# Optimization experiments

Hardware: AMD Instinct MI355X
Metric: run time of the kernel (lower is better)

The kernel has to match this reference:

```python
import jax, jax.numpy as jnp
import numpy as np

D_MODEL = 512
N_HEAD = 8
D_FF = 2048
HEAD = D_MODEL // N_HEAD
B, S = 2, 4096
LN_EPS = 1e-5


def _layernorm(x, g, b):
    mu = jnp.mean(x, axis=-1, keepdims=True)
    var = jnp.mean(jnp.square(x - mu), axis=-1, keepdims=True)
    return (x - mu) * jax.lax.rsqrt(var + LN_EPS) * g + b


def setup_inputs() -> dict:
    key = jax.random.key(0)
    ks = jax.random.split(key, 12)
    s = 0.02
    inp = {
        "src": jax.random.normal(ks[0], (B, S, D_MODEL), dtype=jnp.float32),
        "mask": jnp.ones((B, S, S), dtype=jnp.float32),
        "Wq": jax.random.normal(ks[1], (D_MODEL, D_MODEL), dtype=jnp.float32) * s,
        "bq": jnp.zeros((D_MODEL,), dtype=jnp.float32),
        "Wk": jax.random.normal(ks[2], (D_MODEL, D_MODEL), dtype=jnp.float32) * s,
        "bk": jnp.zeros((D_MODEL,), dtype=jnp.float32),
        "Wv": jax.random.normal(ks[3], (D_MODEL, D_MODEL), dtype=jnp.float32) * s,
        "bv": jnp.zeros((D_MODEL,), dtype=jnp.float32),
        "Wo": jax.random.normal(ks[4], (D_MODEL, D_MODEL), dtype=jnp.float32) * s,
        "bo": jnp.zeros((D_MODEL,), dtype=jnp.float32),
        "W1": jax.random.normal(ks[5], (D_FF, D_MODEL), dtype=jnp.float32) * s,
        "b1": jnp.zeros((D_FF,), dtype=jnp.float32),
        "W2": jax.random.normal(ks[6], (D_MODEL, D_FF), dtype=jnp.float32) * s,
        "b2": jnp.zeros((D_MODEL,), dtype=jnp.float32),
        "ln1_g": jnp.ones((D_MODEL,), dtype=jnp.float32),
        "ln1_b": jnp.zeros((D_MODEL,), dtype=jnp.float32),
        "ln2_g": jnp.ones((D_MODEL,), dtype=jnp.float32),
        "ln2_b": jnp.zeros((D_MODEL,), dtype=jnp.float32),
    }
    return inp


def reference(src, mask, Wq, bq, Wk, bk, Wv, bv, Wo, bo, W1, b1, W2, b2,
              ln1_g, ln1_b, ln2_g, ln2_b):
    # --- multi-head self-attention (chunk/cat == head split on last dim) ---
    def heads(x, W, b):
        y = x @ W.T + b  # [B,S,D]
        return y.reshape(B, S, N_HEAD, HEAD)
    Q = heads(src, Wq, bq)
    K = heads(src, Wk, bk)
    V = heads(src, Wv, bv)
    score = jnp.einsum('bihd,bjhd->bhij', Q, K) / jnp.sqrt(jnp.float32(HEAD))
    score = score + ((1.0 - mask) * -1e9)[:, None, :, :]
    attn = jax.nn.softmax(score, axis=-1)
    ctx = jnp.einsum('bhij,bjhd->bihd', attn, V).reshape(B, S, D_MODEL)
    sa = ctx @ Wo.T + bo
    # --- residual + LN1 ---
    x = _layernorm(src + sa, ln1_g, ln1_b)
    # --- FFN (relu) + residual + LN2 ---
    ff = jax.nn.relu(x @ W1.T + b1) @ W2.T + b2
    return _layernorm(x + ff, ln2_g, ln2_b)
```

## Files before the change

### kernel.cpp

```cpp
#include <hip/hip_runtime.h>
#include <cstdint>
#include <cstddef>

#define DM   512
#define SQL  4096
#define NHE  8
#define HDM  64
#define DFF  2048
#define NB   2

typedef unsigned short u16t;
typedef __attribute__((ext_vector_type(8))) __bf16 bf16x8;
typedef __attribute__((ext_vector_type(4))) float f32x4;
typedef __attribute__((ext_vector_type(8))) unsigned short us8;
typedef __attribute__((ext_vector_type(4))) unsigned short us4;
typedef __attribute__((ext_vector_type(4))) short s16x4;

extern "C" __device__ float __ocml_native_exp2_f32(float);
__device__ inline float ex2(float x) { return __ocml_native_exp2_f32(x); }

__device__ inline f32x4 mfma16(bf16x8 a, bf16x8 b, f32x4 c) {
    return __builtin_amdgcn_mfma_f32_16x16x32_bf16(a, b, c, 0, 0, 0);
}
__device__ inline f32x4 mfma16k16(s16x4 a, s16x4 b, f32x4 c) {
    return __builtin_amdgcn_mfma_f32_16x16x16bf16_1k(a, b, c, 0, 0, 0);
}

__device__ inline void load_lds16(const void* g, void* l) {
    __builtin_amdgcn_global_load_lds(
        (const __attribute__((address_space(1))) unsigned int*)g,
        (__attribute__((address_space(3))) unsigned int*)l, 16, 0, 0);
}

__device__ inline u16t f2bf(float x) {
    union { float f; unsigned int u; } v; v.f = x;
    unsigned int r = v.u + 0x7fffu + ((v.u >> 16) & 1u);
    return (u16t)(r >> 16);
}

__device__ inline unsigned int pk_bf2(float lo, float hi) {
    union { float f; unsigned int u; } a, b;
    a.f = lo; b.f = hi;
    return __builtin_amdgcn_perm(b.u + 0x8000u, a.u + 0x8000u, 0x07060302u);
}

__device__ inline void store_out(float* C, size_t idx, float v) { C[idx] = v; }
__device__ inline void store_out(u16t* C, size_t idx, float v) { C[idx] = f2bf(v); }

__global__ __launch_bounds__(256) void convert_all(
    const float* __restrict__ src, const float* __restrict__ Wq,
    const float* __restrict__ Wk, const float* __restrict__ Wv,
    const float* __restrict__ Wo, const float* __restrict__ W1,
    const float* __restrict__ W2, const float* __restrict__ bq,
    const float* __restrict__ bk, const float* __restrict__ bv,
    const f32x4* __restrict__ mask4,
    u16t* __restrict__ srcbf, u16t* __restrict__ wqkv, u16t* __restrict__ woc,
    u16t* __restrict__ w1c, u16t* __restrict__ w2c,
    float* __restrict__ bqkv, int* __restrict__ flag) {
    const int blk = blockIdx.x;
    const float* s;
    u16t* d;
    int base;
    if (blk < 2048)      { s = src; d = srcbf;           base = blk; }
    else if (blk < 2176) { s = Wq;  d = wqkv;            base = blk - 2048; }
    else if (blk < 2304) { s = Wk;  d = wqkv + 262144;   base = blk - 2176; }
    else if (blk < 2432) { s = Wv;  d = wqkv + 524288;   base = blk - 2304; }
    else if (blk < 2560) { s = Wo;  d = woc;             base = blk - 2432; }
    else if (blk < 3072) { s = W1;  d = w1c;             base = blk - 2560; }
    else if (blk < 3584) { s = W2;  d = w2c;             base = blk - 3072; }
    else if (blk == 3584) {
        for (int i = threadIdx.x; i < 1536; i += 256)
            bqkv[i] = (i < 512) ? bq[i] : (i < 1024 ? bk[i - 512] : bv[i - 1024]);
        return;
    } else {
        const size_t n4 = (size_t)NB * SQL * SQL / 4;
        size_t i = (size_t)(blk - 3585) * 256 + threadIdx.x;
        bool bad = false;
        for (; i < n4; i += (size_t)2048 * 256) {
            f32x4 v = mask4[i];
            bad |= (v[0] != 1.0f) || (v[1] != 1.0f) || (v[2] != 1.0f) || (v[3] != 1.0f);
        }
        if (bad) flag[0] = 42;
        return;
    }
    const int i = base * 2048 + threadIdx.x * 8;
    f32x4 a = *(const f32x4*)(s + i);
    f32x4 b = *(const f32x4*)(s + i + 4);
    us8 o;
    o[0] = f2bf(a[0]); o[1] = f2bf(a[1]); o[2] = f2bf(a[2]); o[3] = f2bf(a[3]);
    o[4] = f2bf(b[0]); o[5] = f2bf(b[1]); o[6] = f2bf(b[2]); o[7] = f2bf(b[3]);
    *(us8*)(d + i) = o;
}

template <typename OutT, bool RELU, int BN>
__global__ __launch_bounds__(256, 3) void gemm_bt(const u16t* __restrict__ A,
                                                  const u16t* __restrict__ Bw,
                                                  const float* __restrict__ bias,
                                                  OutT* __restrict__ C,
                                                  const int M, const int N, const int K,
                                                  const int ldc) {
    __shared__ u16t As[128 * 32];
    __shared__ u16t Bs[BN * 32];
    constexpr int NT = BN / 32;
    const int tid = threadIdx.x;
    const int w = tid >> 6, lane = tid & 63;
    const int l15 = lane & 15, quad = lane >> 4;
    const int m0 = blockIdx.y * 128, n0 = blockIdx.x * BN;
    const int wm = w >> 1, wn = w & 1;

    f32x4 acc[4][NT] = {};

    const u16t* Ag = A + ((size_t)(m0 + w * 32 + (lane >> 2))) * K + (lane & 3) * 8;
    const u16t* Bg = Bw + ((size_t)(n0 + w * (BN / 4) + (lane >> 2))) * K + (lane & 3) * 8;
    u16t* Asw = &As[(w * 32) * 32];
    u16t* Bsw = &Bs[(w * (BN / 4)) * 32];

    for (int k0 = 0; k0 < K; k0 += 32) {
        __syncthreads();
        load_lds16(Ag + k0, Asw);
        load_lds16(Ag + (size_t)16 * K + k0, Asw + 16 * 32);
#pragma unroll
        for (int i = 0; i < BN / 64; ++i)
            load_lds16(Bg + (size_t)(16 * i) * K + k0, Bsw + i * 16 * 32);
        __syncthreads();
        bf16x8 af[4], bfr[NT];
#pragma unroll
        for (int mt = 0; mt < 4; ++mt)
            af[mt] = *(const bf16x8*)&As[(wm * 64 + mt * 16 + l15) * 32 + quad * 8];
#pragma unroll
        for (int nt = 0; nt < NT; ++nt)
            bfr[nt] = *(const bf16x8*)&Bs[(wn * (BN / 2) + nt * 16 + l15) * 32 + quad * 8];
#pragma unroll
        for (int mt = 0; mt < 4; ++mt)
#pragma unroll
            for (int nt = 0; nt < NT; ++nt)
                acc[mt][nt] = mfma16(af[mt], bfr[nt], acc[mt][nt]);
    }

    float bv[NT];
#pragma unroll
    for (int nt = 0; nt < NT; ++nt) bv[nt] = bias[n0 + wn * (BN / 2) + nt * 16 + l15];
#pragma unroll
    for (int mt = 0; mt < 4; ++mt)
#pragma unroll
        for (int r = 0; r < 4; ++r) {
            const int row = m0 + wm * 64 + mt * 16 + quad * 4 + r;
#pragma unroll
            for (int nt = 0; nt < NT; ++nt) {
                float v = acc[mt][nt][r] + bv[nt];
                if (RELU) v = fmaxf(v, 0.0f);
                store_out(C, (size_t)row * ldc + n0 + wn * (BN / 2) + nt * 16 + l15, v);
            }
        }
}

__global__ __launch_bounds__(256) void transpose_v(const u16t* __restrict__ qkv,
                                                   u16t* __restrict__ vt) {
    __shared__ u16t t[64 * 72];
    const int sb = blockIdx.x, h = blockIdx.y, b = blockIdx.z;
    const int tid = threadIdx.x;
#pragma unroll
    for (int it = 0; it < 2; ++it) {
        const int idx = it * 256 + tid;
        const int r = idx >> 3, c8 = idx & 7;
        const u16t* gp = qkv + (size_t)(b * SQL + sb * 64 + r) * (3 * DM) + 2 * DM + h * HDM + c8 * 8;
        *(us8*)&t[r * 72 + c8 * 8] = *(const us8*)gp;
    }
    __syncthreads();
#pragma unroll
    for (int it = 0; it < 2; ++it) {
        const int idx = it * 256 + tid;
        const int d = idx >> 3, s8 = idx & 7;
        us8 o;
#pragma unroll
        for (int u = 0; u < 8; ++u) o[u] = t[(s8 * 8 + u) * 72 + d];
        u16t* gp = vt + (size_t)((b * NHE + h) * HDM + d) * SQL + sb * 64 + s8 * 8;
        *(us8*)gp = o;
    }
}

__global__ __launch_bounds__(256, 2) void flash_attn(const u16t* __restrict__ qkv,
                                                     const u16t* __restrict__ vtg,
                                                     const float* __restrict__ mask,
                                                     const int* __restrict__ flag,
                                                     u16t* __restrict__ ctx) {
    __shared__ u16t Ks[128 * 64];
    __shared__ u16t Vs[64 * 128];

    const int qt = blockIdx.x, h = blockIdx.y, b = blockIdx.z;
    const int tid = threadIdx.x;
    const int w = tid >> 6, lane = tid & 63;
    const int l15 = lane & 15, quad = lane >> 4;
    const int e3 = l15 & 7;
    const bool allones = (*flag != 42);

    bf16x8 qf[2][2];
#pragma unroll
    for (int mt = 0; mt < 2; ++mt) {
        const size_t rowb = (size_t)(b * SQL + qt * 128 + w * 32 + mt * 16 + l15) * (3 * DM) + h * HDM;
#pragma unroll
        for (int kk = 0; kk < 2; ++kk)
            qf[mt][kk] = *(const bf16x8*)(qkv + rowb + kk * 32 + quad * 8);
    }

    f32x4 oacc[4][2] = {};
    float m_r[2] = {-3.0e38f, -3.0e38f};
    float l_r[2] = {0.0f, 0.0f};

    const int r8 = lane >> 3, c8 = lane & 7;
    const int r4 = lane >> 4, c16 = lane & 15;

    for (int kt = 0; kt < SQL / 128; ++kt) {
        const int j0 = kt * 128;
        __syncthreads();
#pragma unroll
        for (int i = 0; i < 4; ++i) {
            const int row = j0 + w * 32 + i * 8 + r8;
            load_lds16(qkv + (size_t)(b * SQL + row) * (3 * DM) + DM + h * HDM + ((c8 ^ r8) * 8),
                       &Ks[(w * 32 + i * 8) * 64]);
        }
#pragma unroll
        for (int i = 0; i < 4; ++i) {
            const int d = w * 16 + i * 4 + r4;
            load_lds16(vtg + (size_t)((b * NHE + h) * HDM + d) * SQL + j0 + ((c16 ^ ((i * 4 + r4) & 7)) * 8),
                       &Vs[(w * 16 + i * 4) * 128]);
        }
        __syncthreads();

        f32x4 sacc[2][8] = {};
#pragma unroll
        for (int kk = 0; kk < 2; ++kk) {
#pragma unroll
            for (int jt = 0; jt < 8; ++jt) {
                bf16x8 af = *(const bf16x8*)&Ks[(jt * 16 + l15) * 64 + (((kk * 4 + quad) ^ e3) * 8)];
                sacc[0][jt] = mfma16(af, qf[0][kk], sacc[0][jt]);
                sacc[1][jt] = mfma16(af, qf[1][kk], sacc[1][jt]);
            }
        }

        float av[2][4];
#pragma unroll
        for (int mt = 0; mt < 2; ++mt) {
            if (!allones) {
                const int gi = qt * 128 + w * 32 + mt * 16 + l15;
#pragma unroll
                for (int jt = 0; jt < 8; ++jt)
#pragma unroll
                    for (int r = 0; r < 4; ++r) {
                        const int gj = j0 + jt * 16 + quad * 4 + r;
                        sacc[mt][jt][r] = sacc[mt][jt][r] * 0.125f
                                        + (1.0f - mask[((size_t)b * SQL + gi) * SQL + gj]) * (-1.0e9f);
                    }
            }
            float mx = -3.0e38f;
#pragma unroll
            for (int jt = 0; jt < 8; ++jt)
#pragma unroll
                for (int r = 0; r < 4; ++r) mx = fmaxf(mx, sacc[mt][jt][r]);
            mx = fmaxf(mx, __shfl_xor(mx, 16));
            mx = fmaxf(mx, __shfl_xor(mx, 32));
            const float cs = allones ? 0.18033688011112042f : 1.4426950408889634f;
            const float mnew = fmaxf(m_r[mt], mx);
            const float mb = mnew * cs;
            const float alpha = ex2(fmaf(m_r[mt], cs, -mb));
            m_r[mt] = mnew;
            float rsum = 0.0f;
#pragma unroll
            for (int jt = 0; jt < 8; ++jt)
#pragma unroll
                for (int r = 0; r < 4; ++r) {
                    const float p = ex2(fmaf(sacc[mt][jt][r], cs, -mb));
                    sacc[mt][jt][r] = p;
                    rsum += p;
                }
            rsum += __shfl_xor(rsum, 16);
            rsum += __shfl_xor(rsum, 32);
            l_r[mt] = l_r[mt] * alpha + rsum;
#pragma unroll
            for (int r = 0; r < 4; ++r) av[mt][r] = __shfl(alpha, quad * 4 + r);
#pragma unroll
            for (int dt = 0; dt < 4; ++dt)
#pragma unroll
                for (int r = 0; r < 4; ++r) oacc[dt][mt][r] *= av[mt][r];
        }

#pragma unroll
        for (int jt = 0; jt < 8; ++jt) {
            union { s16x4 v; unsigned int u[2]; } pa0, pa1;
            pa0.u[0] = pk_bf2(sacc[0][jt][0], sacc[0][jt][1]);
            pa0.u[1] = pk_bf2(sacc[0][jt][2], sacc[0][jt][3]);
            pa1.u[0] = pk_bf2(sacc[1][jt][0], sacc[1][jt][1]);
            pa1.u[1] = pk_bf2(sacc[1][jt][2], sacc[1][jt][3]);
            const int vcol = (((2 * jt + (quad >> 1)) ^ e3) * 8) + (quad & 1) * 4;
#pragma unroll
            for (int dt = 0; dt < 4; ++dt) {
                s16x4 vb = *(const s16x4*)&Vs[(dt * 16 + l15) * 128 + vcol];
                oacc[dt][0] = mfma16k16(pa0.v, vb, oacc[dt][0]);
                oacc[dt][1] = mfma16k16(pa1.v, vb, oacc[dt][1]);
            }
        }
    }

#pragma unroll
    for (int mt = 0; mt < 2; ++mt) {
        float lv[4];
#pragma unroll
        for (int r = 0; r < 4; ++r) lv[r] = __shfl(l_r[mt], quad * 4 + r);
#pragma unroll
        for (int r = 0; r < 4; ++r) {
            const float inv = 1.0f / lv[r];
            const int token = qt * 128 + w * 32 + mt * 16 + quad * 4 + r;
            const size_t base = (size_t)(b * SQL + token) * DM + h * HDM;
#pragma unroll
            for (int dt = 0; dt < 4; ++dt)
                ctx[base + dt * 16 + l15] = f2bf(oacc[dt][mt][r] * inv);
        }
    }
}

template <bool WBF>
__global__ __launch_bounds__(256) void ln_fused(const float* __restrict__ xa,
                                                const float* __restrict__ xb,
                                                const float* __restrict__ g,
                                                const float* __restrict__ be,
                                                float* __restrict__ outf,
                                                u16t* __restrict__ outh) {
    const int row = blockIdx.x * 4 + (threadIdx.x >> 6);
    const int lane = threadIdx.x & 63;
    const size_t base = (size_t)row * DM;
    f32x4 a0 = *(const f32x4*)(xa + base + lane * 4);
    f32x4 b0 = *(const f32x4*)(xb + base + lane * 4);
    f32x4 a1 = *(const f32x4*)(xa + base + 256 + lane * 4);
    f32x4 b1 = *(const f32x4*)(xb + base + 256 + lane * 4);
    f32x4 v0 = a0 + b0, v1 = a1 + b1;
    float s = v0[0] + v0[1] + v0[2] + v0[3] + v1[0] + v1[1] + v1[2] + v1[3];
    float q = v0[0]*v0[0] + v0[1]*v0[1] + v0[2]*v0[2] + v0[3]*v0[3]
            + v1[0]*v1[0] + v1[1]*v1[1] + v1[2]*v1[2] + v1[3]*v1[3];
#pragma unroll
    for (int off = 1; off < 64; off <<= 1) {
        s += __shfl_xor(s, off);
        q += __shfl_xor(q, off);
    }
    const float mean = s * (1.0f / DM);
    const float var = q * (1.0f / DM) - mean * mean;
    const float rs = rsqrtf(var + 1e-5f);
    f32x4 g0 = *(const f32x4*)(g + lane * 4);
    f32x4 g1 = *(const f32x4*)(g + 256 + lane * 4);
    f32x4 e0 = *(const f32x4*)(be + lane * 4);
    f32x4 e1 = *(const f32x4*)(be + 256 + lane * 4);
    f32x4 y0, y1;
#pragma unroll
    for (int i = 0; i < 4; ++i) {
        y0[i] = (v0[i] - mean) * rs * g0[i] + e0[i];
        y1[i] = (v1[i] - mean) * rs * g1[i] + e1[i];
    }
    *(f32x4*)(outf + base + lane * 4) = y0;
    *(f32x4*)(outf + base + 256 + lane * 4) = y1;
    if (WBF) {
        us4 h0, h1;
#pragma unroll
        for (int i = 0; i < 4; ++i) { h0[i] = f2bf(y0[i]); h1[i] = f2bf(y1[i]); }
        *(us4*)(outh + base + lane * 4) = h0;
        *(us4*)(outh + base + 256 + lane * 4) = h1;
    }
}

extern "C" void kernel_launch(void* const* d_in, const int* in_sizes, int n_in,
                              void* d_out, int out_size, void* d_ws, size_t ws_size,
                              hipStream_t stream) {
    const float* src  = (const float*)d_in[0];
    const float* mask = (const float*)d_in[1];
    const float* Wq = (const float*)d_in[2];
    const float* bq = (const float*)d_in[3];
    const float* Wk = (const float*)d_in[4];
    const float* bk = (const float*)d_in[5];
    const float* Wv = (const float*)d_in[6];
    const float* bv = (const float*)d_in[7];
    const float* Wo = (const float*)d_in[8];
    const float* bo = (const float*)d_in[9];
    const float* W1 = (const float*)d_in[10];
    const float* b1 = (const float*)d_in[11];
    const float* W2 = (const float*)d_in[12];
    const float* b2 = (const float*)d_in[13];
    const float* ln1g = (const float*)d_in[14];
    const float* ln1b = (const float*)d_in[15];
    const float* ln2g = (const float*)d_in[16];
    const float* ln2b = (const float*)d_in[17];

    const int M = NB * SQL;

    char* p = (char*)d_ws;
    auto take = [&](size_t bytes) {
        char* r = p;
        p += (bytes + 1023) & ~(size_t)1023;
        return r;
    };
    u16t* regA   = (u16t*)take((size_t)M * DFF * 2);
    u16t* vtb    = (u16t*)take((size_t)NB * NHE * HDM * SQL * 2);
    u16t* ctxb   = (u16t*)take((size_t)M * DM * 2);
    float* sa_ff = (float*)take((size_t)M * DM * 4);
    float* x1f   = (float*)take((size_t)M * DM * 4);
    u16t* x1h    = (u16t*)take((size_t)M * DM * 2);
    u16t* srcbf  = (u16t*)take((size_t)M * DM * 2);
    u16t* wqkv   = (u16t*)take((size_t)3 * DM * DM * 2);
    float* bqkv  = (float*)take((size_t)3 * DM * 4);
    u16t* woc    = (u16t*)take((size_t)DM * DM * 2);
    u16t* w1c    = (u16t*)take((size_t)DFF * DM * 2);
    u16t* w2c    = (u16t*)take((size_t)DM * DFF * 2);
    int* flag    = (int*)take(1024);
    u16t* qkvb   = regA;
    u16t* hbuf   = regA;

    convert_all<<<5633, 256, 0, stream>>>(src, Wq, Wk, Wv, Wo, W1, W2, bq, bk, bv,
                                          (const f32x4*)mask,
                                          srcbf, wqkv, woc, w1c, w2c, bqkv, flag);

    gemm_bt<u16t, false, 128><<<dim3(12, 64), 256, 0, stream>>>(srcbf, wqkv, bqkv, qkvb,
                                                                M, 3 * DM, DM, 3 * DM);
    transpose_v<<<dim3(SQL / 64, NHE, NB), 256, 0, stream>>>(qkvb, vtb);
    flash_attn<<<dim3(SQL / 128, NHE, NB), 256, 0, stream>>>(qkvb, vtb, mask, flag, ctxb);
    gemm_bt<float, false, 64><<<dim3(8, 64), 256, 0, stream>>>(ctxb, woc, bo, sa_ff,
                                                               M, DM, DM, DM);
    ln_fused<true><<<M / 4, 256, 0, stream>>>(src, sa_ff, ln1g, ln1b, x1f, x1h);
    gemm_bt<u16t, true, 128><<<dim3(16, 64), 256, 0, stream>>>(x1h, w1c, b1, hbuf,
                                                               M, DFF, DM, DFF);
    gemm_bt<float, false, 64><<<dim3(8, 64), 256, 0, stream>>>(hbuf, w2c, b2, sa_ff,
                                                               M, DM, DFF, DM);
    ln_fused<false><<<M / 4, 256, 0, stream>>>(x1f, sa_ff, ln2g, ln2b, (float*)d_out,
                                               (u16t*)nullptr);
}
```

Measured before the change: 471.4 us.

## Double-buffer K/V tiles in flash attention and deepen GEMM K-tile to 64

The flash attention kernel now keeps two LDS buffers for K and V. It prefetches the next 128-key tile while computing on the current one, which removes one barrier per iteration and overlaps global loads with MFMA work. The GEMM K-step grows from 32 to 64, with an XOR-swizzled LDS layout to avoid bank conflicts. This halves the barrier count per K. LDS use roughly doubles in both kernels, which may limit occupancy.

```diff
diff --git a/kernel.cpp b/kernel.cpp
--- a/kernel.cpp
+++ b/kernel.cpp
@@ -99,42 +99,51 @@
                                                   OutT* __restrict__ C,
                                                   const int M, const int N, const int K,
                                                   const int ldc) {
-    __shared__ u16t As[128 * 32];
-    __shared__ u16t Bs[BN * 32];
+    __shared__ u16t As[128 * 64];
+    __shared__ u16t Bs[BN * 64];
     constexpr int NT = BN / 32;
     const int tid = threadIdx.x;
     const int w = tid >> 6, lane = tid & 63;
     const int l15 = lane & 15, quad = lane >> 4;
+    const int e3 = l15 & 7;
     const int m0 = blockIdx.y * 128, n0 = blockIdx.x * BN;
     const int wm = w >> 1, wn = w & 1;
 
     f32x4 acc[4][NT] = {};
 
-    const u16t* Ag = A + ((size_t)(m0 + w * 32 + (lane >> 2))) * K + (lane & 3) * 8;
-    const u16t* Bg = Bw + ((size_t)(n0 + w * (BN / 4) + (lane >> 2))) * K + (lane & 3) * 8;
-    u16t* Asw = &As[(w * 32) * 32];
-    u16t* Bsw = &Bs[(w * (BN / 4)) * 32];
-
-    for (int k0 = 0; k0 < K; k0 += 32) {
+    const int r8 = lane >> 3;
+    const int c8s = ((lane & 7) ^ r8) * 8;
+    const u16t* Ag = A + (size_t)(m0 + w * 32 + r8) * K + c8s;
+    const u16t* Bg = Bw + (size_t)(n0 + w * (BN / 4) + r8) * K + c8s;
+    u16t* Asw = &As[(w * 32) * 64];
+    u16t* Bsw = &Bs[(w * (BN / 4)) * 64];
+
+    for (int k0 = 0; k0 < K; k0 += 64) {
         __syncthreads();
-        load_lds16(Ag + k0, Asw);
-        load_lds16(Ag + (size_t)16 * K + k0, Asw + 16 * 32);
-#pragma unroll
-        for (int i = 0; i < BN / 64; ++i)
-            load_lds16(Bg + (size_t)(16 * i) * K + k0, Bsw + i * 16 * 32);
+#pragma unroll
+        for (int i = 0; i < 4; ++i)
+            load_lds16(Ag + (size_t)(i * 8) * K + k0, Asw + i * 8 * 64);
+#pragma unroll
+        for (int i = 0; i < BN / 32; ++i)
+            load_lds16(Bg + (size_t)(i * 8) * K + k0, Bsw + i * 8 * 64);
         __syncthreads();
-        bf16x8 af[4], bfr[NT];
-#pragma unroll
-        for (int mt = 0; mt < 4; ++mt)
-            af[mt] = *(const bf16x8*)&As[(wm * 64 + mt * 16 + l15) * 32 + quad * 8];
-#pragma unroll
-        for (int nt = 0; nt < NT; ++nt)
-            bfr[nt] = *(const bf16x8*)&Bs[(wn * (BN / 2) + nt * 16 + l15) * 32 + quad * 8];
-#pragma unroll
-        for (int mt = 0; mt < 4; ++mt)
+#pragma unroll
+        for (int kk = 0; kk < 2; ++kk) {
+            bf16x8 af[4], bfr[NT];
+#pragma unroll
+            for (int mt = 0; mt < 4; ++mt)
+                af[mt] = *(const bf16x8*)&As[(wm * 64 + mt * 16 + l15) * 64
+                                             + (((kk * 4 + quad) ^ e3) * 8)];
 #pragma unroll
             for (int nt = 0; nt < NT; ++nt)
-                acc[mt][nt] = mfma16(af[mt], bfr[nt], acc[mt][nt]);
+                bfr[nt] = *(const bf16x8*)&Bs[(wn * (BN / 2) + nt * 16 + l15) * 64
+                                              + (((kk * 4 + quad) ^ e3) * 8)];
+#pragma unroll
+            for (int mt = 0; mt < 4; ++mt)
+#pragma unroll
+                for (int nt = 0; nt < NT; ++nt)
+                    acc[mt][nt] = mfma16(af[mt], bfr[nt], acc[mt][nt]);
+        }
     }
 
     float bv[NT];
@@ -184,8 +193,8 @@
                                                      const float* __restrict__ mask,
                                                      const int* __restrict__ flag,
                                                      u16t* __restrict__ ctx) {
-    __shared__ u16t Ks[128 * 64];
-    __shared__ u16t Vs[64 * 128];
+    __shared__ u16t Ks[2][128 * 64];
+    __shared__ u16t Vs[2][64 * 128];
 
     const int qt = blockIdx.x, h = blockIdx.y, b = blockIdx.z;
     const int tid = threadIdx.x;
@@ -193,6 +202,12 @@
     const int l15 = lane & 15, quad = lane >> 4;
     const int e3 = l15 & 7;
     const bool allones = (*flag != 42);
+    const float cs = allones ? 0.18033688011112042f : 1.4426950408889634f;
+
+    const int r8 = lane >> 3, c8 = lane & 7;
+    const int r4 = lane >> 4, c16 = lane & 15;
+    const u16t* Kg = qkv + (size_t)b * SQL * (3 * DM) + DM + h * HDM;
+    const u16t* Vg = vtg + (size_t)(b * NHE + h) * HDM * SQL;
 
     bf16x8 qf[2][2];
 #pragma unroll
@@ -207,32 +222,37 @@
     float m_r[2] = {-3.0e38f, -3.0e38f};
     float l_r[2] = {0.0f, 0.0f};
 
-    const int r8 = lane >> 3, c8 = lane & 7;
-    const int r4 = lane >> 4, c16 = lane & 15;
+#pragma unroll
+    for (int i = 0; i < 4; ++i)
+        load_lds16(Kg + (size_t)(w * 32 + i * 8 + r8) * (3 * DM) + ((c8 ^ r8) * 8),
+                   &Ks[0][(w * 32 + i * 8) * 64]);
+#pragma unroll
+    for (int i = 0; i < 4; ++i)
+        load_lds16(Vg + (size_t)(w * 16 + i * 4 + r4) * SQL + ((c16 ^ ((i * 4 + r4) & 7)) * 8),
+                   &Vs[0][(w * 16 + i * 4) * 128]);
 
     for (int kt = 0; kt < SQL / 128; ++kt) {
+        const int cur = kt & 1;
         const int j0 = kt * 128;
         __syncthreads();
-#pragma unroll
-        for (int i = 0; i < 4; ++i) {
-            const int row = j0 + w * 32 + i * 8 + r8;
-            load_lds16(qkv + (size_t)(b * SQL + row) * (3 * DM) + DM + h * HDM + ((c8 ^ r8) * 8),
-                       &Ks[(w * 32 + i * 8) * 64]);
-        }
-#pragma unroll
-        for (int i = 0; i < 4; ++i) {
-            const int d = w * 16 + i * 4 + r4;
-            load_lds16(vtg + (size_t)((b * NHE + h) * HDM + d) * SQL + j0 + ((c16 ^ ((i * 4 + r4) & 7)) * 8),
-                       &Vs[(w * 16 + i * 4) * 128]);
-        }
-        __syncthreads();
+        if (kt + 1 < SQL / 128) {
+            const int j1 = j0 + 128;
+#pragma unroll
+            for (int i = 0; i < 4; ++i)
+                load_lds16(Kg + (size_t)(j1 + w * 32 + i * 8 + r8) * (3 * DM) + ((c8 ^ r8) * 8),
+                           &Ks[cur ^ 1][(w * 32 + i * 8) * 64]);
+#pragma unroll
+            for (int i = 0; i < 4; ++i)
+                load_lds16(Vg + (size_t)(w * 16 + i * 4 + r4) * SQL + j1 + ((c16 ^ ((i * 4 + r4) & 7)) * 8),
+                           &Vs[cur ^ 1][(w * 16 + i * 4) * 128]);
+        }
 
         f32x4 sacc[2][8] = {};
 #pragma unroll
         for (int kk = 0; kk < 2; ++kk) {
 #pragma unroll
             for (int jt = 0; jt < 8; ++jt) {
-                bf16x8 af = *(const bf16x8*)&Ks[(jt * 16 + l15) * 64 + (((kk * 4 + quad) ^ e3) * 8)];
+                bf16x8 af = *(const bf16x8*)&Ks[cur][(jt * 16 + l15) * 64 + (((kk * 4 + quad) ^ e3) * 8)];
                 sacc[0][jt] = mfma16(af, qf[0][kk], sacc[0][jt]);
                 sacc[1][jt] = mfma16(af, qf[1][kk], sacc[1][jt]);
             }
@@ -259,7 +279,6 @@
                 for (int r = 0; r < 4; ++r) mx = fmaxf(mx, sacc[mt][jt][r]);
             mx = fmaxf(mx, __shfl_xor(mx, 16));
             mx = fmaxf(mx, __shfl_xor(mx, 32));
-            const float cs = allones ? 0.18033688011112042f : 1.4426950408889634f;
             const float mnew = fmaxf(m_r[mt], mx);
             const float mb = mnew * cs;
             const float alpha = ex2(fmaf(m_r[mt], cs, -mb));
@@ -294,7 +313,7 @@
             const int vcol = (((2 * jt + (quad >> 1)) ^ e3) * 8) + (quad & 1) * 4;
 #pragma unroll
             for (int dt = 0; dt < 4; ++dt) {
-                s16x4 vb = *(const s16x4*)&Vs[(dt * 16 + l15) * 128 + vcol];
+                s16x4 vb = *(const s16x4*)&Vs[cur][(dt * 16 + l15) * 128 + vcol];
                 oacc[dt][0] = mfma16k16(pa0.v, vb, oacc[dt][0]);
                 oacc[dt][1] = mfma16k16(pa1.v, vb, oacc[dt][1]);
             }
```

Measured after the change: 477.0 us. About the same (+1.2%).
